# Kernel tuning notes

Measured on AMD Instinct MI355X. Metric: run time of the kernel, lower is better.

Reference implementation:

```python
import jax, jax.numpy as jnp
import numpy as np

B, S, H, NSPANS, NCLS = 32, 4096, 1024, 16, 25
MAX_SPAN_LEN = 64


def setup_inputs() -> dict:
    key = jax.random.key(0)
    k_emb, k_w1, k_b1, k_w2, k_b2 = jax.random.split(key, 5)
    all_emb = jax.random.normal(k_emb, (B, S, H), dtype=jnp.float32)

    # Build span table with (0,0) padding after the first n_valid spans
    # (the torch code breaks on the first (0,0) row).
    rng = np.random.default_rng(0)
    starts = rng.integers(1, S - MAX_SPAN_LEN, size=(B, NSPANS))
    lengths = rng.integers(1, MAX_SPAN_LEN, size=(B, NSPANS))
    ends = starts + lengths
    spans = np.stack([starts, ends], axis=-1).astype(np.int32)  # [B,N,2]
    n_valid = rng.integers(1, NSPANS + 1, size=(B,))
    for i in range(B):
        spans[i, n_valid[i]:, :] = 0
    sp_token_positions = jnp.asarray(spans)

    sc1 = 1.0 / np.sqrt(H)
    W1 = jax.random.normal(k_w1, (H, H), dtype=jnp.float32) * sc1
    b1 = jax.random.normal(k_b1, (H,), dtype=jnp.float32) * 0.01
    W2 = jax.random.normal(k_w2, (H, NCLS), dtype=jnp.float32) * sc1
    b2 = jax.random.normal(k_b2, (NCLS,), dtype=jnp.float32) * 0.01
    return {"all_emb": all_emb, "sp_token_positions": sp_token_positions,
            "W1": W1, "b1": b1, "W2": W2, "b2": b2}


def _span_mean(all_emb, spans):
    # spans: [B, N, 2] int32. A span is valid only if it is non-(0,0) AND all
    # earlier spans in its row are valid (torch 'break' semantics).
    s0 = spans[..., 0]  # [B,N]
    s1 = spans[..., 1]
    nonzero = ((s0 != 0) | (s1 != 0)).astype(jnp.float32)
    valid = jnp.cumprod(nonzero, axis=1)  # [B,N]

    t = jnp.arange(all_emb.shape[1])  # [S]
    # in_span[b,n,t] = start <= t < end; overlapping spans count tokens twice,
    # exactly like the torch.cat-then-mean original.
    in_span = ((t[None, None, :] >= s0[..., None]) &
               (t[None, None, :] < s1[..., None])).astype(jnp.float32)
    weights = jnp.einsum('bnt,bn->bt', in_span, valid)  # [B,S] token counts
    total = jnp.sum(weights, axis=1, keepdims=True)     # [B,1]
    summed = jnp.einsum('bsh,bs->bh', all_emb, weights)  # [B,H]
    return summed / total


def reference(all_emb, sp_token_positions, W1, b1, W2, b2):
    pooled = _span_mean(all_emb, sp_token_positions)        # [B,H]
    h = jax.nn.relu(pooled @ W1 + b1)                       # fc1 + relu
    logits = h @ W2 + b2                                    # fc2
    return jax.nn.sigmoid(logits)                           # [B,25]
```

## Files before the change

kernel.cpp:

```cpp
#include <hip/hip_runtime.h>
#include <math.h>

#define B      32
#define S      4096
#define H      1024
#define NSPANS 16
#define NCLS   25

__global__ __launch_bounds__(256) void span_pool_kernel(
    const float* __restrict__ emb,
    const int*   __restrict__ spans,
    float*       __restrict__ pooled)
{
    const int n = blockIdx.x;
    const int b = blockIdx.y;

    __shared__ int   sh_s0, sh_s1, sh_valid;
    __shared__ float sh_scale;

    if (threadIdx.x == 0) {
        int total = 0, valid = 0, s0 = 0, s1 = 0;
        for (int k = 0; k < NSPANS; ++k) {
            int a = spans[(b * NSPANS + k) * 2 + 0];
            int e = spans[(b * NSPANS + k) * 2 + 1];
            if (a == 0 && e == 0) break;
            total += (e - a);
            if (k == n) { valid = 1; s0 = a; s1 = e; }
        }
        sh_valid = valid;
        sh_s0 = s0;
        sh_s1 = s1;
        sh_scale = (total > 0) ? (1.0f / (float)total) : 0.0f;
    }
    __syncthreads();

    if (!sh_valid) return;
    const int   s0    = sh_s0;
    const int   s1    = sh_s1;
    const float scale = sh_scale;

    const float4* base = (const float4*)(emb + (size_t)b * S * H);
    const int hv = threadIdx.x;

    float4 acc = make_float4(0.f, 0.f, 0.f, 0.f);
    for (int t = s0; t < s1; ++t) {
        float4 v = base[(size_t)t * (H / 4) + hv];
        acc.x += v.x; acc.y += v.y; acc.z += v.z; acc.w += v.w;
    }

    float* dst = pooled + (size_t)b * H + hv * 4;
    atomicAdd(dst + 0, acc.x * scale);
    atomicAdd(dst + 1, acc.y * scale);
    atomicAdd(dst + 2, acc.z * scale);
    atomicAdd(dst + 3, acc.w * scale);
}

__global__ __launch_bounds__(256) void fc1_relu_kernel(
    const float* __restrict__ pooled,
    const float* __restrict__ W1,
    const float* __restrict__ b1,
    float*       __restrict__ hbuf)
{
    const int b  = blockIdx.x >> 2;
    const int j  = ((blockIdx.x & 3) << 8) + threadIdx.x;

    __shared__ float pool_s[H];
    const float4* src  = (const float4*)(pooled + (size_t)b * H);
    float4*       dst4 = (float4*)pool_s;
    dst4[threadIdx.x] = src[threadIdx.x];
    __syncthreads();

    float acc = b1[j];
    const float* w = W1 + j;
    #pragma unroll 8
    for (int i = 0; i < H; ++i) {
        acc = fmaf(pool_s[i], w[(size_t)i * H], acc);
    }
    hbuf[(size_t)b * H + j] = fmaxf(acc, 0.0f);
}

__global__ __launch_bounds__(256) void fc2_sigmoid_kernel(
    const float* __restrict__ hbuf,
    const float* __restrict__ W2,
    const float* __restrict__ b2,
    float*       __restrict__ out)
{
    const int c = blockIdx.x;
    const int b = blockIdx.y;

    const float* hrow = hbuf + (size_t)b * H;
    float partial = 0.0f;
    #pragma unroll
    for (int i = threadIdx.x; i < H; i += 256) {
        partial = fmaf(hrow[i], W2[(size_t)i * NCLS + c], partial);
    }

    #pragma unroll
    for (int off = 32; off > 0; off >>= 1)
        partial += __shfl_down(partial, off, 64);

    __shared__ float wsum[4];
    const int wave = threadIdx.x >> 6;
    const int lane = threadIdx.x & 63;
    if (lane == 0) wsum[wave] = partial;
    __syncthreads();

    if (threadIdx.x == 0) {
        float s = wsum[0] + wsum[1] + wsum[2] + wsum[3] + b2[c];
        out[(size_t)b * NCLS + c] = 1.0f / (1.0f + expf(-s));
    }
}

extern "C" void kernel_launch(void* const* d_in, const int* in_sizes, int n_in,
                              void* d_out, int out_size, void* d_ws, size_t ws_size,
                              hipStream_t stream) {
    const float* emb   = (const float*)d_in[0];
    const int*   spans = (const int*)  d_in[1];
    const float* W1    = (const float*)d_in[2];
    const float* b1    = (const float*)d_in[3];
    const float* W2    = (const float*)d_in[4];
    const float* b2    = (const float*)d_in[5];
    float*       out   = (float*)d_out;

    float* pooled = (float*)d_ws;
    float* hbuf   = pooled + B * H;

    hipMemsetAsync(d_ws, 0, (size_t)B * H * sizeof(float), stream);

    span_pool_kernel<<<dim3(NSPANS, B), 256, 0, stream>>>(emb, spans, pooled);
    fc1_relu_kernel<<<dim3(B * 4), 256, 0, stream>>>(pooled, W1, b1, hbuf);
    fc2_sigmoid_kernel<<<dim3(NCLS, B), 256, 0, stream>>>(hbuf, W2, b2, out);
}
```

Before: 672.4 us.

## Parallelize span header scan, unroll span accumulation, split fc1 K across waves

The span header scan, previously done serially by one thread, now uses a 64-lane wave with a ballot to find the first (0,0) span and a shuffle reduction for the total length. The span sum loop is unrolled by four with independent accumulators so more loads are in flight per thread. fc1 launches four times as many blocks: each block covers 64 outputs and its four waves each take a quarter of the K dimension, combined through shared memory. This raises parallelism in the latency-bound fc1 GEMV (128 blocks before) at the cost of narrower 256-byte W1 row accesses per wave and an extra barrier.

```diff
diff --git a/kernel.cpp b/kernel.cpp
--- a/kernel.cpp
+++ b/kernel.cpp
@@ -18,19 +18,26 @@
     __shared__ int   sh_s0, sh_s1, sh_valid;
     __shared__ float sh_scale;
 
-    if (threadIdx.x == 0) {
-        int total = 0, valid = 0, s0 = 0, s1 = 0;
-        for (int k = 0; k < NSPANS; ++k) {
-            int a = spans[(b * NSPANS + k) * 2 + 0];
-            int e = spans[(b * NSPANS + k) * 2 + 1];
-            if (a == 0 && e == 0) break;
-            total += (e - a);
-            if (k == n) { valid = 1; s0 = a; s1 = e; }
+    if (threadIdx.x < 64) {
+        const int k = threadIdx.x;
+        int a = 0, e = 0;
+        if (k < NSPANS) {
+            a = spans[(b * NSPANS + k) * 2 + 0];
+            e = spans[(b * NSPANS + k) * 2 + 1];
         }
-        sh_valid = valid;
-        sh_s0 = s0;
-        sh_s1 = s1;
-        sh_scale = (total > 0) ? (1.0f / (float)total) : 0.0f;
+        unsigned long long nzmask = __ballot((a | e) != 0);
+        const int nvalid = (int)__builtin_ctzll(~nzmask);
+
+        int len = (k < nvalid) ? (e - a) : 0;
+        #pragma unroll
+        for (int off = 32; off > 0; off >>= 1)
+            len += __shfl_down(len, off, 64);
+
+        if (k == 0) {
+            sh_scale = (len > 0) ? (1.0f / (float)len) : 0.0f;
+            sh_valid = (n < nvalid);
+        }
+        if (k == n) { sh_s0 = a; sh_s1 = e; }
     }
     __syncthreads();
 
@@ -39,20 +46,39 @@
     const int   s1    = sh_s1;
     const float scale = sh_scale;
 
-    const float4* base = (const float4*)(emb + (size_t)b * S * H);
-    const int hv = threadIdx.x;
+    const float4* base = (const float4*)(emb + (size_t)b * S * H) + threadIdx.x;
 
-    float4 acc = make_float4(0.f, 0.f, 0.f, 0.f);
-    for (int t = s0; t < s1; ++t) {
-        float4 v = base[(size_t)t * (H / 4) + hv];
-        acc.x += v.x; acc.y += v.y; acc.z += v.z; acc.w += v.w;
+    float4 a0 = make_float4(0.f, 0.f, 0.f, 0.f);
+    float4 a1 = make_float4(0.f, 0.f, 0.f, 0.f);
+    float4 a2 = make_float4(0.f, 0.f, 0.f, 0.f);
+    float4 a3 = make_float4(0.f, 0.f, 0.f, 0.f);
+
+    int t = s0;
+    for (; t + 4 <= s1; t += 4) {
+        float4 v0 = base[(size_t)(t + 0) * (H / 4)];
+        float4 v1 = base[(size_t)(t + 1) * (H / 4)];
+        float4 v2 = base[(size_t)(t + 2) * (H / 4)];
+        float4 v3 = base[(size_t)(t + 3) * (H / 4)];
+        a0.x += v0.x; a0.y += v0.y; a0.z += v0.z; a0.w += v0.w;
+        a1.x += v1.x; a1.y += v1.y; a1.z += v1.z; a1.w += v1.w;
+        a2.x += v2.x; a2.y += v2.y; a2.z += v2.z; a2.w += v2.w;
+        a3.x += v3.x; a3.y += v3.y; a3.z += v3.z; a3.w += v3.w;
+    }
+    for (; t < s1; ++t) {
+        float4 v = base[(size_t)t * (H / 4)];
+        a0.x += v.x; a0.y += v.y; a0.z += v.z; a0.w += v.w;
     }
 
-    float* dst = pooled + (size_t)b * H + hv * 4;
-    atomicAdd(dst + 0, acc.x * scale);
-    atomicAdd(dst + 1, acc.y * scale);
-    atomicAdd(dst + 2, acc.z * scale);
-    atomicAdd(dst + 3, acc.w * scale);
+    a0.x += a1.x + a2.x + a3.x;
+    a0.y += a1.y + a2.y + a3.y;
+    a0.z += a1.z + a2.z + a3.z;
+    a0.w += a1.w + a2.w + a3.w;
+
+    float* dst = pooled + (size_t)b * H + threadIdx.x * 4;
+    atomicAdd(dst + 0, a0.x * scale);
+    atomicAdd(dst + 1, a0.y * scale);
+    atomicAdd(dst + 2, a0.z * scale);
+    atomicAdd(dst + 3, a0.w * scale);
 }
 
 __global__ __launch_bounds__(256) void fc1_relu_kernel(
@@ -61,22 +87,34 @@
     const float* __restrict__ b1,
     float*       __restrict__ hbuf)
 {
-    const int b  = blockIdx.x >> 2;
-    const int j  = ((blockIdx.x & 3) << 8) + threadIdx.x;
+    const int b    = blockIdx.x >> 4;
+    const int jblk = (blockIdx.x & 15) << 6;
+    const int lane = threadIdx.x & 63;
+    const int quad = threadIdx.x >> 6;
+    const int j    = jblk + lane;
 
     __shared__ float pool_s[H];
-    const float4* src  = (const float4*)(pooled + (size_t)b * H);
-    float4*       dst4 = (float4*)pool_s;
-    dst4[threadIdx.x] = src[threadIdx.x];
+    ((float4*)pool_s)[threadIdx.x] =
+        ((const float4*)(pooled + (size_t)b * H))[threadIdx.x];
     __syncthreads();
 
-    float acc = b1[j];
     const float* w = W1 + j;
+    float acc = 0.0f;
+    const int i0 = quad * (H / 4);
     #pragma unroll 8
-    for (int i = 0; i < H; ++i) {
+    for (int i = i0; i < i0 + H / 4; ++i) {
         acc = fmaf(pool_s[i], w[(size_t)i * H], acc);
     }
-    hbuf[(size_t)b * H + j] = fmaxf(acc, 0.0f);
+
+    __shared__ float part[4][64];
+    part[quad][lane] = acc;
+    __syncthreads();
+
+    if (threadIdx.x < 64) {
+        float s = part[0][lane] + part[1][lane] + part[2][lane] + part[3][lane]
+                + b1[jblk + lane];
+        hbuf[(size_t)b * H + jblk + lane] = fmaxf(s, 0.0f);
+    }
 }
 
 __global__ __launch_bounds__(256) void fc2_sigmoid_kernel(
@@ -128,6 +166,6 @@
     hipMemsetAsync(d_ws, 0, (size_t)B * H * sizeof(float), stream);
 
     span_pool_kernel<<<dim3(NSPANS, B), 256, 0, stream>>>(emb, spans, pooled);
-    fc1_relu_kernel<<<dim3(B * 4), 256, 0, stream>>>(pooled, W1, b1, hbuf);
+    fc1_relu_kernel<<<dim3(B * 16), 256, 0, stream>>>(pooled, W1, b1, hbuf);
     fc2_sigmoid_kernel<<<dim3(NCLS, B), 256, 0, stream>>>(hbuf, W2, b2, out);
 }
```

Result: faster. 610.1 us (-9.3%).
